# Kernel optimization log

Measured on AMD Instinct MI355X. Metric: run time of the kernel, lower is better.

The kernel has to match this reference:

```python
import jax, jax.numpy as jnp
import numpy as np

B, T, E, H = 256, 256, 384, 64

def setup_inputs() -> dict:
    key = jax.random.key(0)
    ks = jax.random.split(key, 4)
    s = 1.0 / np.sqrt(E)
    return {
        "x":  jax.random.normal(ks[0], (B, T, E), dtype=jnp.float32),
        "Wq": jax.random.normal(ks[1], (E, H), dtype=jnp.float32) * s,
        "bq": jnp.zeros((H,), dtype=jnp.float32),
        "Wk": jax.random.normal(ks[2], (E, H), dtype=jnp.float32) * s,
        "bk": jnp.zeros((H,), dtype=jnp.float32),
        "Wv": jax.random.normal(ks[3], (E, H), dtype=jnp.float32) * s,
        "bv": jnp.zeros((H,), dtype=jnp.float32),
    }

def reference(x, Wq, bq, Wk, bk, Wv, bv):
    # QKV projections: [B,T,E] @ [E,H] -> [B,T,H]
    q = x @ Wq + bq
    k = x @ Wk + bk
    v = x @ Wv + bv
    # attention scores (NOTE: original has no 1/sqrt(d) scaling)
    wei = jnp.einsum('bth,bsh->bts', q, k)  # [B,T,T]
    causal = jnp.tril(jnp.ones((T, T), dtype=bool))
    wei = jnp.where(causal, wei, -jnp.inf)
    wei = jax.nn.softmax(wei, axis=-1)
    # dropout is identity in eval mode
    out = jnp.einsum('bts,bsh->bth', wei, v)  # [B,T,H]
    return out
```

## Files before the change

kernel.cpp:

```cpp
#include <hip/hip_runtime.h>
#include <math.h>

#define Bb 256
#define Tt 256
#define Ee 384
#define Hh 64

typedef __attribute__((ext_vector_type(8))) short bf16x8;
typedef __attribute__((ext_vector_type(4))) float f32x4;
typedef __attribute__((ext_vector_type(4))) unsigned int u32x4;

__device__ inline short f2bf(float f) {
    unsigned u = __float_as_uint(f);
    u += 0x7FFFu + ((u >> 16) & 1);
    return (short)(u >> 16);
}
__device__ inline float bf2f(short s) {
    return __uint_as_float(((unsigned)(unsigned short)s) << 16);
}
__device__ inline unsigned cvt_pk_bf16(float a, float b) {
    unsigned r;
    asm("v_cvt_pk_bf16_f32 %0, %1, %2" : "=v"(r) : "v"(a), "v"(b));
    return r;
}

#define MFMA16(a, b, c) __builtin_amdgcn_mfma_f32_16x16x32_bf16((a), (b), (c), 0, 0, 0)

#define WLO_OFF 147456

#define BB0 65536
#define K_HI 0
#define K_LO 32768
#define VF   65536
#define QH   98304
#define QL   116736
#define PBASE 98304
#define SMEM_BYTES 135168

__global__ __launch_bounds__(256) void prep_w(
    const float* __restrict__ Wq, const float* __restrict__ Wk,
    const float* __restrict__ Wv, unsigned char* __restrict__ wsp)
{
    int u = blockIdx.x * 256 + threadIdx.x;
    if (u >= 9216) return;
    int frag = u >> 6;
    int lu   = u & 63;
    int ec   = frag / 12, tct = frag - ec * 12;
    int koct = lu >> 4, n = lu & 15;
    int col  = tct * 16 + n;
    const float* Wm = (col < 64) ? Wq : ((col < 128) ? Wk : Wv);
    int c = col & 63;
    bf16x8 hi8, lo8;
    #pragma unroll
    for (int j = 0; j < 8; ++j) {
        float v = Wm[(ec * 32 + koct * 8 + j) * 64 + c];
        short h = f2bf(v);
        hi8[j] = h;
        lo8[j] = f2bf(v - bf2f(h));
    }
    *reinterpret_cast<bf16x8*>(wsp + frag * 1024 + lu * 16) = hi8;
    *reinterpret_cast<bf16x8*>(wsp + WLO_OFF + frag * 1024 + lu * 16) = lo8;
}

__global__ __launch_bounds__(1024) void head_fused(
    const float* __restrict__ x,
    const float* __restrict__ bq, const float* __restrict__ bk,
    const float* __restrict__ bv,
    const unsigned char* __restrict__ wsp,
    float* __restrict__ out)
{
    __shared__ __align__(16) unsigned char smem[SMEM_BYTES];

    const int b    = blockIdx.x;
    const int tid  = threadIdx.x;
    const int w    = tid >> 6;
    const int lane = tid & 63;
    const int quad = lane >> 4;
    const int nl   = lane & 15;
    const int ri   = w >> 2;
    const int cj   = w & 3;

    f32x4 acc[4][3];
    #pragma unroll
    for (int i = 0; i < 4; ++i)
        #pragma unroll
        for (int j = 0; j < 3; ++j) acc[i][j] = (f32x4){0,0,0,0};

    const float4* x4 = reinterpret_cast<const float4*>(x + (size_t)b * Tt * Ee);

    auto bgld = [&](int ecn) {
        if (w < 12) {
            int p = ecn & 1;
            const unsigned char* ghi = wsp + (size_t)(ecn * 12 + w) * 1024 + (size_t)lane * 16;
            const unsigned char* glo = ghi + WLO_OFF;
            __builtin_amdgcn_global_load_lds(
                (const __attribute__((address_space(1))) unsigned*)ghi,
                (__attribute__((address_space(3))) unsigned*)(smem + BB0 + p * 24576 + w * 1024),
                16, 0, 0);
            __builtin_amdgcn_global_load_lds(
                (const __attribute__((address_space(1))) unsigned*)glo,
                (__attribute__((address_space(3))) unsigned*)(smem + BB0 + p * 24576 + 12288 + w * 1024),
                16, 0, 0);
        }
    };

    const int pt = tid & 255;
    const float4* xp = x4 + pt * 96;
    unsigned char* adst = smem + (pt >> 4) * 1024 + (pt & 15) * 16;

    auto stageA = [&](int ecsrc, int nb) {
        float4 px[8];
        const float4* xr_ = xp + ecsrc * 8;
        #pragma unroll
        for (int j = 0; j < 8; ++j) px[j] = xr_[j];
        #pragma unroll
        for (int ko = 0; ko < 4; ++ko) {
            float v0 = px[2*ko+0].x, v1 = px[2*ko+0].y,
                  v2 = px[2*ko+0].z, v3 = px[2*ko+0].w,
                  v4 = px[2*ko+1].x, v5 = px[2*ko+1].y,
                  v6 = px[2*ko+1].z, v7 = px[2*ko+1].w;
            unsigned h0 = cvt_pk_bf16(v0, v1);
            unsigned h1 = cvt_pk_bf16(v2, v3);
            unsigned h2 = cvt_pk_bf16(v4, v5);
            unsigned h3 = cvt_pk_bf16(v6, v7);
            unsigned l0 = cvt_pk_bf16(v0 - __uint_as_float(h0 << 16),
                                      v1 - __uint_as_float(h0 & 0xFFFF0000u));
            unsigned l1 = cvt_pk_bf16(v2 - __uint_as_float(h1 << 16),
                                      v3 - __uint_as_float(h1 & 0xFFFF0000u));
            unsigned l2 = cvt_pk_bf16(v4 - __uint_as_float(h2 << 16),
                                      v5 - __uint_as_float(h2 & 0xFFFF0000u));
            unsigned l3 = cvt_pk_bf16(v6 - __uint_as_float(h3 << 16),
                                      v7 - __uint_as_float(h3 & 0xFFFF0000u));
            u32x4 hv = {h0, h1, h2, h3};
            u32x4 lv = {l0, l1, l2, l3};
            *reinterpret_cast<u32x4*>(adst + nb + ko * 256) = hv;
            *reinterpret_cast<u32x4*>(adst + nb + 16384 + ko * 256) = lv;
        }
    };

    bgld(0);
    if (w >= 12) stageA(0, 0);

    for (int ec = 0; ec < 12; ++ec) {
        __syncthreads();
        if (w < 12) {
            if (ec < 11) bgld(ec + 1);
        } else {
            if (ec < 11) stageA(ec + 1, (1 - (ec & 1)) * 32768);
        }

        const int ab = (ec & 1) * 32768;
        const int bb = BB0 + (ec & 1) * 24576;
        bf16x8 bh[3], bl[3];
        #pragma unroll
        for (int ct = 0; ct < 3; ++ct) {
            int o = bb + (cj * 3 + ct) * 1024 + lane * 16;
            bh[ct] = *reinterpret_cast<bf16x8*>(smem + o);
            bl[ct] = *reinterpret_cast<bf16x8*>(smem + o + 12288);
        }
        #pragma unroll
        for (int rt = 0; rt < 4; ++rt) {
            int ao = ab + (4 * ri + rt) * 1024 + lane * 16;
            bf16x8 ah = *reinterpret_cast<bf16x8*>(smem + ao);
            bf16x8 al = *reinterpret_cast<bf16x8*>(smem + ao + 16384);
            #pragma unroll
            for (int ct = 0; ct < 3; ++ct) {
                acc[rt][ct] = MFMA16(ah, bh[ct], acc[rt][ct]);
                acc[rt][ct] = MFMA16(al, bh[ct], acc[rt][ct]);
                acc[rt][ct] = MFMA16(ah, bl[ct], acc[rt][ct]);
            }
        }
    }
    __syncthreads();

    #pragma unroll
    for (int ct = 0; ct < 3; ++ct) {
        int col = (cj * 3 + ct) * 16 + nl;
        float bias = (col < 64) ? bq[col] : (col < 128 ? bk[col - 64] : bv[col - 128]);
        #pragma unroll
        for (int rt = 0; rt < 4; ++rt)
            #pragma unroll
            for (int r = 0; r < 4; ++r) acc[rt][ct][r] += bias;
    }

    #pragma unroll
    for (int ct = 0; ct < 3; ++ct) {
        int col = (cj * 3 + ct) * 16 + nl;
        #pragma unroll
        for (int rt = 0; rt < 4; ++rt) {
            #pragma unroll
            for (int r = 0; r < 4; ++r) {
                float val = acc[rt][ct][r];
                int s = ri * 64 + rt * 16 + quad * 4 + r;
                if (col >= 64 && col < 128) {
                    int h = col - 64;
                    int addr = ((s >> 4) * 2 + (h >> 5)) * 1024
                             + ((((h & 31) >> 3) * 16 + (s & 15)) * 8 + (h & 7)) * 2;
                    short hi = f2bf(val);
                    short lo = f2bf(val - bf2f(hi));
                    *reinterpret_cast<short*>(smem + K_HI + addr) = hi;
                    *reinterpret_cast<short*>(smem + K_LO + addr) = lo;
                } else if (col >= 128) {
                    int h = col - 128, sl = s & 31;
                    int addr = ((s >> 5) * 4 + (h >> 4)) * 1024
                             + (((sl >> 3) * 16 + (h & 15)) * 8 + (sl & 7)) * 2;
                    *reinterpret_cast<short*>(smem + VF + addr) = f2bf(val);
                }
            }
        }
    }

    auto writeQhalf = [&]() {
        #pragma unroll
        for (int ct = 0; ct < 3; ++ct) {
            int col = (cj * 3 + ct) * 16 + nl;
            if (col < 64) {
                #pragma unroll
                for (int rt = 0; rt < 4; ++rt) {
                    #pragma unroll
                    for (int r = 0; r < 4; ++r) {
                        float val = acc[rt][ct][r];
                        int s = ri * 64 + rt * 16 + quad * 4 + r;
                        int rloc = s & 127;
                        short hi = f2bf(val);
                        short lo = f2bf(val - bf2f(hi));
                        *reinterpret_cast<short*>(smem + QH + (rloc * 72 + col) * 2) = hi;
                        *reinterpret_cast<short*>(smem + QL + (rloc * 72 + col) * 2) = lo;
                    }
                }
            }
        }
    };
    bf16x8 qh0, qh1, ql0, ql1;
    auto readQ = [&]() {
        int rloc = (16 * w + nl) & 127;
        int base = rloc * 144;
        qh0 = *reinterpret_cast<bf16x8*>(smem + QH + base + quad * 16);
        qh1 = *reinterpret_cast<bf16x8*>(smem + QH + base + 64 + quad * 16);
        ql0 = *reinterpret_cast<bf16x8*>(smem + QL + base + quad * 16);
        ql1 = *reinterpret_cast<bf16x8*>(smem + QL + base + 64 + quad * 16);
    };

    if (ri < 2) writeQhalf();
    __syncthreads();
    if (w < 8) readQ();
    __syncthreads();
    if (ri >= 2) writeQhalf();
    __syncthreads();
    if (w >= 8) readQ();
    __syncthreads();

    f32x4 oacc[4];
    #pragma unroll
    for (int i = 0; i < 4; ++i) oacc[i] = (f32x4){0,0,0,0};
    float lsum = 0.f;
    const int t0 = w * 16;
    unsigned char* pb = smem + PBASE + w * 1344;
    const int npairs = (w >> 1) + 1;

    for (int p = 0; p < npairs; ++p) {
        #pragma unroll
        for (int hf = 0; hf < 2; ++hf) {
            int st = 2 * p + hf;
            f32x4 s0 = (f32x4){0,0,0,0}, s1 = (f32x4){0,0,0,0};
            int kb = st * 2048 + lane * 16;
            bf16x8 kh0 = *reinterpret_cast<bf16x8*>(smem + K_HI + kb);
            bf16x8 kh1 = *reinterpret_cast<bf16x8*>(smem + K_HI + kb + 1024);
            bf16x8 kl0 = *reinterpret_cast<bf16x8*>(smem + K_LO + kb);
            bf16x8 kl1 = *reinterpret_cast<bf16x8*>(smem + K_LO + kb + 1024);
            s0 = MFMA16(qh0, kh0, s0);
            s1 = MFMA16(qh1, kh1, s1);
            s0 = MFMA16(ql0, kh0, s0);
            s1 = MFMA16(ql1, kh1, s1);
            s0 = MFMA16(qh0, kl0, s0);
            s1 = MFMA16(qh1, kl1, s1);
            int sg = st * 16 + nl;
            #pragma unroll
            for (int r = 0; r < 4; ++r) {
                int tg = t0 + quad * 4 + r;
                float sv = s0[r] + s1[r];
                float pv = (sg <= tg) ? __expf(sv) : 0.f;
                *reinterpret_cast<short*>(pb + ((quad * 4 + r) * 40 + hf * 16 + nl) * 2) = f2bf(pv);
            }
        }
        asm volatile("s_waitcnt lgkmcnt(0)" ::: "memory");
        bf16x8 pa = *reinterpret_cast<bf16x8*>(pb + (nl * 40 + quad * 8) * 2);
        float ls = 0.f;
        #pragma unroll
        for (int j = 0; j < 8; ++j) ls += bf2f(pa[j]);
        ls += __shfl_xor(ls, 16);
        ls += __shfl_xor(ls, 32);
        lsum += ls;
        int vb = p * 4096 + lane * 16;
        #pragma unroll
        for (int nt = 0; nt < 4; ++nt) {
            bf16x8 vf = *reinterpret_cast<bf16x8*>(smem + VF + vb + nt * 1024);
            oacc[nt] = MFMA16(pa, vf, oacc[nt]);
        }
    }

    float* lb_ = reinterpret_cast<float*>(pb + 1280);
    if (lane < 16) lb_[lane] = lsum;
    asm volatile("s_waitcnt lgkmcnt(0)" ::: "memory");
    float* ob = out + (size_t)b * Tt * Hh + (size_t)t0 * Hh;
    #pragma unroll
    for (int r = 0; r < 4; ++r) {
        float inv = 1.0f / lb_[quad * 4 + r];
        #pragma unroll
        for (int nt = 0; nt < 4; ++nt)
            ob[(quad * 4 + r) * 64 + nt * 16 + nl] = oacc[nt][r] * inv;
    }
}

extern "C" void kernel_launch(void* const* d_in, const int* in_sizes, int n_in,
                              void* d_out, int out_size, void* d_ws, size_t ws_size,
                              hipStream_t stream) {
    const float* x  = (const float*)d_in[0];
    const float* Wq = (const float*)d_in[1];
    const float* bq = (const float*)d_in[2];
    const float* bk = (const float*)d_in[4];
    const float* Wk = (const float*)d_in[3];
    const float* Wv = (const float*)d_in[5];
    const float* bv = (const float*)d_in[6];
    float* out = (float*)d_out;
    unsigned char* wsp = (unsigned char*)d_ws;
    hipLaunchKernelGGL(prep_w, dim3(36), dim3(256), 0, stream, Wq, Wk, Wv, wsp);
    hipLaunchKernelGGL(head_fused, dim3(Bb), dim3(1024), 0, stream,
                       x, bq, bk, bv, wsp, out);
}
```

Before: 186.3 us.

## Prefetch x one stage ahead, raise MFMA priority, compute softmax sums in registers

Splits the A-staging step into a global load and a convert/write so the producer waves issue the x loads for chunk ec+2 while chunk ec is consumed, hiding global latency. Wraps MFMA blocks in s_setprio to favour matrix issue across waves. Computes softmax row sums from the fp32 probabilities with cross-lane shuffles instead of re-reading the bf16 P tile and storing sums through LDS. This adds register pressure from the held prefetch buffer, and the normaliser now uses unrounded values.

```diff
diff --git a/kernel.cpp b/kernel.cpp
--- a/kernel.cpp
+++ b/kernel.cpp
@@ -107,12 +107,14 @@
     const int pt = tid & 255;
     const float4* xp = x4 + pt * 96;
     unsigned char* adst = smem + (pt >> 4) * 1024 + (pt & 15) * 16;
-
-    auto stageA = [&](int ecsrc, int nb) {
-        float4 px[8];
+    float4 px[8];
+
+    auto loadX = [&](int ecsrc) {
         const float4* xr_ = xp + ecsrc * 8;
         #pragma unroll
         for (int j = 0; j < 8; ++j) px[j] = xr_[j];
+    };
+    auto stageWrite = [&](int nb) {
         #pragma unroll
         for (int ko = 0; ko < 4; ++ko) {
             float v0 = px[2*ko+0].x, v1 = px[2*ko+0].y,
@@ -139,14 +141,19 @@
     };
 
     bgld(0);
-    if (w >= 12) stageA(0, 0);
+    if (w >= 12) {
+        loadX(0);
+        stageWrite(0);
+        loadX(1);
+    }
 
     for (int ec = 0; ec < 12; ++ec) {
         __syncthreads();
         if (w < 12) {
             if (ec < 11) bgld(ec + 1);
         } else {
-            if (ec < 11) stageA(ec + 1, (1 - (ec & 1)) * 32768);
+            if (ec < 11) stageWrite((1 - (ec & 1)) * 32768);
+            if (ec < 10) loadX(ec + 2);
         }
 
         const int ab = (ec & 1) * 32768;
@@ -158,6 +165,7 @@
             bh[ct] = *reinterpret_cast<bf16x8*>(smem + o);
             bl[ct] = *reinterpret_cast<bf16x8*>(smem + o + 12288);
         }
+        __builtin_amdgcn_s_setprio(1);
         #pragma unroll
         for (int rt = 0; rt < 4; ++rt) {
             int ao = ab + (4 * ri + rt) * 1024 + lane * 16;
@@ -170,6 +178,7 @@
                 acc[rt][ct] = MFMA16(ah, bl[ct], acc[rt][ct]);
             }
         }
+        __builtin_amdgcn_s_setprio(0);
     }
     __syncthreads();
 
@@ -253,12 +262,13 @@
     f32x4 oacc[4];
     #pragma unroll
     for (int i = 0; i < 4; ++i) oacc[i] = (f32x4){0,0,0,0};
-    float lsum = 0.f;
+    float lsum4[4] = {0.f, 0.f, 0.f, 0.f};
     const int t0 = w * 16;
     unsigned char* pb = smem + PBASE + w * 1344;
     const int npairs = (w >> 1) + 1;
 
     for (int p = 0; p < npairs; ++p) {
+        float rs[4] = {0.f, 0.f, 0.f, 0.f};
         #pragma unroll
         for (int hf = 0; hf < 2; ++hf) {
             int st = 2 * p + hf;
@@ -268,44 +278,49 @@
             bf16x8 kh1 = *reinterpret_cast<bf16x8*>(smem + K_HI + kb + 1024);
             bf16x8 kl0 = *reinterpret_cast<bf16x8*>(smem + K_LO + kb);
             bf16x8 kl1 = *reinterpret_cast<bf16x8*>(smem + K_LO + kb + 1024);
+            __builtin_amdgcn_s_setprio(1);
             s0 = MFMA16(qh0, kh0, s0);
             s1 = MFMA16(qh1, kh1, s1);
             s0 = MFMA16(ql0, kh0, s0);
             s1 = MFMA16(ql1, kh1, s1);
             s0 = MFMA16(qh0, kl0, s0);
             s1 = MFMA16(qh1, kl1, s1);
+            __builtin_amdgcn_s_setprio(0);
             int sg = st * 16 + nl;
             #pragma unroll
             for (int r = 0; r < 4; ++r) {
                 int tg = t0 + quad * 4 + r;
                 float sv = s0[r] + s1[r];
                 float pv = (sg <= tg) ? __expf(sv) : 0.f;
+                rs[r] += pv;
                 *reinterpret_cast<short*>(pb + ((quad * 4 + r) * 40 + hf * 16 + nl) * 2) = f2bf(pv);
             }
         }
+        #pragma unroll
+        for (int r = 0; r < 4; ++r) {
+            float v = rs[r];
+            v += __shfl_xor(v, 1);
+            v += __shfl_xor(v, 2);
+            v += __shfl_xor(v, 4);
+            v += __shfl_xor(v, 8);
+            lsum4[r] += v;
+        }
         asm volatile("s_waitcnt lgkmcnt(0)" ::: "memory");
         bf16x8 pa = *reinterpret_cast<bf16x8*>(pb + (nl * 40 + quad * 8) * 2);
-        float ls = 0.f;
-        #pragma unroll
-        for (int j = 0; j < 8; ++j) ls += bf2f(pa[j]);
-        ls += __shfl_xor(ls, 16);
-        ls += __shfl_xor(ls, 32);
-        lsum += ls;
         int vb = p * 4096 + lane * 16;
+        __builtin_amdgcn_s_setprio(1);
         #pragma unroll
         for (int nt = 0; nt < 4; ++nt) {
             bf16x8 vf = *reinterpret_cast<bf16x8*>(smem + VF + vb + nt * 1024);
             oacc[nt] = MFMA16(pa, vf, oacc[nt]);
         }
-    }
-
-    float* lb_ = reinterpret_cast<float*>(pb + 1280);
-    if (lane < 16) lb_[lane] = lsum;
-    asm volatile("s_waitcnt lgkmcnt(0)" ::: "memory");
+        __builtin_amdgcn_s_setprio(0);
+    }
+
     float* ob = out + (size_t)b * Tt * Hh + (size_t)t0 * Hh;
     #pragma unroll
     for (int r = 0; r < 4; ++r) {
-        float inv = 1.0f / lb_[quad * 4 + r];
+        float inv = 1.0f / lsum4[r];
         #pragma unroll
         for (int nt = 0; nt < 4; ++nt)
             ob[(quad * 4 + r) * 64 + nt * 16 + nl] = oacc[nt][r] * inv;
@@ -318,8 +333,8 @@
     const float* x  = (const float*)d_in[0];
     const float* Wq = (const float*)d_in[1];
     const float* bq = (const float*)d_in[2];
+    const float* Wk = (const float*)d_in[3];
     const float* bk = (const float*)d_in[4];
-    const float* Wk = (const float*)d_in[3];
     const float* Wv = (const float*)d_in[5];
     const float* bv = (const float*)d_in[6];
     float* out = (float*)d_out;
```

New measurement: 188.1 us. Within noise of the previous version (+1.0%).

## Specialize warps into producers and 12 MFMA consumers with 4x4 tiles

Applied to the files above, without the earlier changes.

The projection stage is reorganized so four producer waves handle both the weight global-to-LDS loads and the x fp32-to-bf16 hi/lo staging, while twelve consumer waves each compute a 64x64 tile (4x4 MFMA tiles) for one of Q, K or V. This removes the per-element column branching in the epilogue, packs bf16 conversions with v_cvt_pk_bf16, and raises MFMA priority during compute. prep_w now goes through LDS so its global reads coalesce. The trade-off is that only four waves now stage all of x, so the producer side may become the bottleneck, and each consumer holds more accumulator registers.

```diff
diff --git a/kernel.cpp b/kernel.cpp
--- a/kernel.cpp
+++ b/kernel.cpp
@@ -23,6 +23,8 @@
     asm("v_cvt_pk_bf16_f32 %0, %1, %2" : "=v"(r) : "v"(a), "v"(b));
     return r;
 }
+__device__ inline float lo16f(unsigned u) { return __uint_as_float(u << 16); }
+__device__ inline float hi16f(unsigned u) { return __uint_as_float(u & 0xFFFF0000u); }
 
 #define MFMA16(a, b, c) __builtin_amdgcn_mfma_f32_16x16x32_bf16((a), (b), (c), 0, 0, 0)
 
@@ -41,23 +43,32 @@
     const float* __restrict__ Wq, const float* __restrict__ Wk,
     const float* __restrict__ Wv, unsigned char* __restrict__ wsp)
 {
-    int u = blockIdx.x * 256 + threadIdx.x;
-    if (u >= 9216) return;
-    int frag = u >> 6;
-    int lu   = u & 63;
-    int ec   = frag / 12, tct = frag - ec * 12;
-    int koct = lu >> 4, n = lu & 15;
-    int col  = tct * 16 + n;
-    const float* Wm = (col < 64) ? Wq : ((col < 128) ? Wk : Wv);
-    int c = col & 63;
+    __shared__ float wlds[32 * 66];
+    const int bid = blockIdx.x;
+    const int ec  = bid / 3, m = bid - ec * 3;
+    const float* Wm = (m == 0) ? Wq : (m == 1 ? Wk : Wv);
+    const int tid = threadIdx.x;
+
+    const float4* src = reinterpret_cast<const float4*>(Wm + ec * 2048) + tid * 2;
+    float4 a = src[0], b = src[1];
+    int f = tid * 8;
+    float* d = wlds + (f >> 6) * 66 + (f & 63);
+    d[0] = a.x; d[1] = a.y; d[2] = a.z; d[3] = a.w;
+    d[4] = b.x; d[5] = b.y; d[6] = b.z; d[7] = b.w;
+    __syncthreads();
+
+    const int tl = tid >> 6, lu = tid & 63;
+    const int koct = lu >> 4, n = lu & 15;
+    const int c = tl * 16 + n;
     bf16x8 hi8, lo8;
     #pragma unroll
     for (int j = 0; j < 8; ++j) {
-        float v = Wm[(ec * 32 + koct * 8 + j) * 64 + c];
+        float v = wlds[(koct * 8 + j) * 66 + c];
         short h = f2bf(v);
         hi8[j] = h;
         lo8[j] = f2bf(v - bf2f(h));
     }
+    const int frag = ec * 12 + m * 4 + tl;
     *reinterpret_cast<bf16x8*>(wsp + frag * 1024 + lu * 16) = hi8;
     *reinterpret_cast<bf16x8*>(wsp + WLO_OFF + frag * 1024 + lu * 16) = lo8;
 }
@@ -77,30 +88,31 @@
     const int lane = tid & 63;
     const int quad = lane >> 4;
     const int nl   = lane & 15;
-    const int ri   = w >> 2;
-    const int cj   = w & 3;
-
-    f32x4 acc[4][3];
+    const bool producer = (w >= 12);
+    const int rg   = w & 3;
+    const int cg   = w >> 2;
+
+    f32x4 acc[4][4];
     #pragma unroll
     for (int i = 0; i < 4; ++i)
         #pragma unroll
-        for (int j = 0; j < 3; ++j) acc[i][j] = (f32x4){0,0,0,0};
+        for (int j = 0; j < 4; ++j) acc[i][j] = (f32x4){0,0,0,0};
 
     const float4* x4 = reinterpret_cast<const float4*>(x + (size_t)b * Tt * Ee);
 
     auto bgld = [&](int ecn) {
-        if (w < 12) {
-            int p = ecn & 1;
-            const unsigned char* ghi = wsp + (size_t)(ecn * 12 + w) * 1024 + (size_t)lane * 16;
-            const unsigned char* glo = ghi + WLO_OFF;
+        int p = ecn & 1;
+        int f0 = (w - 12) * 3;
+        #pragma unroll
+        for (int j = 0; j < 3; ++j) {
+            const unsigned char* g = wsp + (size_t)(ecn * 12 + f0 + j) * 1024 + (size_t)lane * 16;
+            unsigned char* dlds = smem + BB0 + p * 24576 + (f0 + j) * 1024;
             __builtin_amdgcn_global_load_lds(
-                (const __attribute__((address_space(1))) unsigned*)ghi,
-                (__attribute__((address_space(3))) unsigned*)(smem + BB0 + p * 24576 + w * 1024),
-                16, 0, 0);
+                (const __attribute__((address_space(1))) unsigned*)g,
+                (__attribute__((address_space(3))) unsigned*)dlds, 16, 0, 0);
             __builtin_amdgcn_global_load_lds(
-                (const __attribute__((address_space(1))) unsigned*)glo,
-                (__attribute__((address_space(3))) unsigned*)(smem + BB0 + p * 24576 + 12288 + w * 1024),
-                16, 0, 0);
+                (const __attribute__((address_space(1))) unsigned*)(g + WLO_OFF),
+                (__attribute__((address_space(3))) unsigned*)(dlds + 12288), 16, 0, 0);
         }
     };
 
@@ -123,14 +135,10 @@
             unsigned h1 = cvt_pk_bf16(v2, v3);
             unsigned h2 = cvt_pk_bf16(v4, v5);
             unsigned h3 = cvt_pk_bf16(v6, v7);
-            unsigned l0 = cvt_pk_bf16(v0 - __uint_as_float(h0 << 16),
-                                      v1 - __uint_as_float(h0 & 0xFFFF0000u));
-            unsigned l1 = cvt_pk_bf16(v2 - __uint_as_float(h1 << 16),
-                                      v3 - __uint_as_float(h1 & 0xFFFF0000u));
-            unsigned l2 = cvt_pk_bf16(v4 - __uint_as_float(h2 << 16),
-                                      v5 - __uint_as_float(h2 & 0xFFFF0000u));
-            unsigned l3 = cvt_pk_bf16(v6 - __uint_as_float(h3 << 16),
-                                      v7 - __uint_as_float(h3 & 0xFFFF0000u));
+            unsigned l0 = cvt_pk_bf16(v0 - lo16f(h0), v1 - hi16f(h0));
+            unsigned l1 = cvt_pk_bf16(v2 - lo16f(h1), v3 - hi16f(h1));
+            unsigned l2 = cvt_pk_bf16(v4 - lo16f(h2), v5 - hi16f(h2));
+            unsigned l3 = cvt_pk_bf16(v6 - lo16f(h3), v7 - hi16f(h3));
             u32x4 hv = {h0, h1, h2, h3};
             u32x4 lv = {l0, l1, l2, l3};
             *reinterpret_cast<u32x4*>(adst + nb + ko * 256) = hv;
@@ -138,96 +146,122 @@
         }
     };
 
-    bgld(0);
-    if (w >= 12) stageA(0, 0);
+    if (producer) {
+        bgld(0);
+        stageA(0, 0);
+    }
 
     for (int ec = 0; ec < 12; ++ec) {
         __syncthreads();
-        if (w < 12) {
-            if (ec < 11) bgld(ec + 1);
+        if (producer) {
+            if (ec < 11) {
+                bgld(ec + 1);
+                stageA(ec + 1, (1 - (ec & 1)) * 32768);
+            }
         } else {
-            if (ec < 11) stageA(ec + 1, (1 - (ec & 1)) * 32768);
-        }
-
-        const int ab = (ec & 1) * 32768;
-        const int bb = BB0 + (ec & 1) * 24576;
-        bf16x8 bh[3], bl[3];
-        #pragma unroll
-        for (int ct = 0; ct < 3; ++ct) {
-            int o = bb + (cj * 3 + ct) * 1024 + lane * 16;
-            bh[ct] = *reinterpret_cast<bf16x8*>(smem + o);
-            bl[ct] = *reinterpret_cast<bf16x8*>(smem + o + 12288);
-        }
-        #pragma unroll
-        for (int rt = 0; rt < 4; ++rt) {
-            int ao = ab + (4 * ri + rt) * 1024 + lane * 16;
-            bf16x8 ah = *reinterpret_cast<bf16x8*>(smem + ao);
-            bf16x8 al = *reinterpret_cast<bf16x8*>(smem + ao + 16384);
-            #pragma unroll
-            for (int ct = 0; ct < 3; ++ct) {
-                acc[rt][ct] = MFMA16(ah, bh[ct], acc[rt][ct]);
-                acc[rt][ct] = MFMA16(al, bh[ct], acc[rt][ct]);
-                acc[rt][ct] = MFMA16(ah, bl[ct], acc[rt][ct]);
-            }
-        }
-    }
-    __syncthreads();
-
-    #pragma unroll
-    for (int ct = 0; ct < 3; ++ct) {
-        int col = (cj * 3 + ct) * 16 + nl;
-        float bias = (col < 64) ? bq[col] : (col < 128 ? bk[col - 64] : bv[col - 128]);
-        #pragma unroll
-        for (int rt = 0; rt < 4; ++rt)
-            #pragma unroll
-            for (int r = 0; r < 4; ++r) acc[rt][ct][r] += bias;
-    }
-
-    #pragma unroll
-    for (int ct = 0; ct < 3; ++ct) {
-        int col = (cj * 3 + ct) * 16 + nl;
-        #pragma unroll
-        for (int rt = 0; rt < 4; ++rt) {
-            #pragma unroll
-            for (int r = 0; r < 4; ++r) {
-                float val = acc[rt][ct][r];
-                int s = ri * 64 + rt * 16 + quad * 4 + r;
-                if (col >= 64 && col < 128) {
-                    int h = col - 64;
-                    int addr = ((s >> 4) * 2 + (h >> 5)) * 1024
-                             + ((((h & 31) >> 3) * 16 + (s & 15)) * 8 + (h & 7)) * 2;
-                    short hi = f2bf(val);
-                    short lo = f2bf(val - bf2f(hi));
-                    *reinterpret_cast<short*>(smem + K_HI + addr) = hi;
-                    *reinterpret_cast<short*>(smem + K_LO + addr) = lo;
-                } else if (col >= 128) {
-                    int h = col - 128, sl = s & 31;
-                    int addr = ((s >> 5) * 4 + (h >> 4)) * 1024
-                             + (((sl >> 3) * 16 + (h & 15)) * 8 + (sl & 7)) * 2;
-                    *reinterpret_cast<short*>(smem + VF + addr) = f2bf(val);
+            const int ab = (ec & 1) * 32768;
+            const int bb = BB0 + (ec & 1) * 24576;
+            bf16x8 bh[4], bl[4];
+            #pragma unroll
+            for (int ct = 0; ct < 4; ++ct) {
+                int o = bb + (cg * 4 + ct) * 1024 + lane * 16;
+                bh[ct] = *reinterpret_cast<bf16x8*>(smem + o);
+                bl[ct] = *reinterpret_cast<bf16x8*>(smem + o + 12288);
+            }
+            __builtin_amdgcn_s_setprio(1);
+            #pragma unroll
+            for (int rt = 0; rt < 4; ++rt) {
+                int ao = ab + (rg * 4 + rt) * 1024 + lane * 16;
+                bf16x8 ah = *reinterpret_cast<bf16x8*>(smem + ao);
+                bf16x8 al = *reinterpret_cast<bf16x8*>(smem + ao + 16384);
+                #pragma unroll
+                for (int ct = 0; ct < 4; ++ct) {
+                    acc[rt][ct] = MFMA16(ah, bh[ct], acc[rt][ct]);
+                    acc[rt][ct] = MFMA16(al, bh[ct], acc[rt][ct]);
+                    acc[rt][ct] = MFMA16(ah, bl[ct], acc[rt][ct]);
                 }
             }
-        }
-    }
-
-    auto writeQhalf = [&]() {
-        #pragma unroll
-        for (int ct = 0; ct < 3; ++ct) {
-            int col = (cj * 3 + ct) * 16 + nl;
-            if (col < 64) {
+            __builtin_amdgcn_s_setprio(0);
+        }
+    }
+    __syncthreads();
+
+    if (!producer) {
+        const float* bias_m = (cg == 0) ? bq : (cg == 1 ? bk : bv);
+        #pragma unroll
+        for (int ct = 0; ct < 4; ++ct) {
+            float bias = bias_m[ct * 16 + nl];
+            #pragma unroll
+            for (int rt = 0; rt < 4; ++rt)
+                #pragma unroll
+                for (int r = 0; r < 4; ++r) acc[rt][ct][r] += bias;
+        }
+
+        if (cg == 1) {
+            #pragma unroll
+            for (int ct = 0; ct < 4; ++ct) {
+                int h = ct * 16 + nl;
                 #pragma unroll
                 for (int rt = 0; rt < 4; ++rt) {
-                    #pragma unroll
-                    for (int r = 0; r < 4; ++r) {
-                        float val = acc[rt][ct][r];
-                        int s = ri * 64 + rt * 16 + quad * 4 + r;
-                        int rloc = s & 127;
-                        short hi = f2bf(val);
-                        short lo = f2bf(val - bf2f(hi));
-                        *reinterpret_cast<short*>(smem + QH + (rloc * 72 + col) * 2) = hi;
-                        *reinterpret_cast<short*>(smem + QL + (rloc * 72 + col) * 2) = lo;
-                    }
+                    f32x4 v = acc[rt][ct];
+                    unsigned h01 = cvt_pk_bf16(v[0], v[1]);
+                    unsigned h23 = cvt_pk_bf16(v[2], v[3]);
+                    unsigned l01 = cvt_pk_bf16(v[0] - lo16f(h01), v[1] - hi16f(h01));
+                    unsigned l23 = cvt_pk_bf16(v[2] - lo16f(h23), v[3] - hi16f(h23));
+                    int a0 = ((rg * 4 + rt) * 2 + (h >> 5)) * 1024
+                           + ((((h & 31) >> 3) * 16 + quad * 4) * 8 + (h & 7)) * 2;
+                    *reinterpret_cast<short*>(smem + K_HI + a0)      = (short)h01;
+                    *reinterpret_cast<short*>(smem + K_HI + a0 + 16) = (short)(h01 >> 16);
+                    *reinterpret_cast<short*>(smem + K_HI + a0 + 32) = (short)h23;
+                    *reinterpret_cast<short*>(smem + K_HI + a0 + 48) = (short)(h23 >> 16);
+                    *reinterpret_cast<short*>(smem + K_LO + a0)      = (short)l01;
+                    *reinterpret_cast<short*>(smem + K_LO + a0 + 16) = (short)(l01 >> 16);
+                    *reinterpret_cast<short*>(smem + K_LO + a0 + 32) = (short)l23;
+                    *reinterpret_cast<short*>(smem + K_LO + a0 + 48) = (short)(l23 >> 16);
                 }
+            }
+        } else if (cg == 2) {
+            #pragma unroll
+            for (int ct = 0; ct < 4; ++ct) {
+                int h = ct * 16 + nl;
+                #pragma unroll
+                for (int rt = 0; rt < 4; ++rt) {
+                    f32x4 v = acc[rt][ct];
+                    unsigned h01 = cvt_pk_bf16(v[0], v[1]);
+                    unsigned h23 = cvt_pk_bf16(v[2], v[3]);
+                    int s29 = rg * 2 + (rt >> 1);
+                    int slh = (rt & 1) * 2 + (quad >> 1);
+                    int sl7 = (quad & 1) * 4;
+                    int a0 = (s29 * 4 + (h >> 4)) * 1024
+                           + ((slh * 16 + (h & 15)) * 8 + sl7) * 2;
+                    *reinterpret_cast<unsigned*>(smem + VF + a0)     = h01;
+                    *reinterpret_cast<unsigned*>(smem + VF + a0 + 4) = h23;
+                }
+            }
+        }
+    }
+
+    auto writeQhalf = [&]() {
+        #pragma unroll
+        for (int ct = 0; ct < 4; ++ct) {
+            int col = ct * 16 + nl;
+            #pragma unroll
+            for (int rt = 0; rt < 4; ++rt) {
+                f32x4 v = acc[rt][ct];
+                unsigned h01 = cvt_pk_bf16(v[0], v[1]);
+                unsigned h23 = cvt_pk_bf16(v[2], v[3]);
+                unsigned l01 = cvt_pk_bf16(v[0] - lo16f(h01), v[1] - hi16f(h01));
+                unsigned l23 = cvt_pk_bf16(v[2] - lo16f(h23), v[3] - hi16f(h23));
+                int s0 = rg * 64 + rt * 16 + quad * 4;
+                int a0 = ((s0 & 127) * 72 + col) * 2;
+                *reinterpret_cast<short*>(smem + QH + a0)       = (short)h01;
+                *reinterpret_cast<short*>(smem + QH + a0 + 144) = (short)(h01 >> 16);
+                *reinterpret_cast<short*>(smem + QH + a0 + 288) = (short)h23;
+                *reinterpret_cast<short*>(smem + QH + a0 + 432) = (short)(h23 >> 16);
+                *reinterpret_cast<short*>(smem + QL + a0)       = (short)l01;
+                *reinterpret_cast<short*>(smem + QL + a0 + 144) = (short)(l01 >> 16);
+                *reinterpret_cast<short*>(smem + QL + a0 + 288) = (short)l23;
+                *reinterpret_cast<short*>(smem + QL + a0 + 432) = (short)(l23 >> 16);
             }
         }
     };
@@ -241,11 +275,11 @@
         ql1 = *reinterpret_cast<bf16x8*>(smem + QL + base + 64 + quad * 16);
     };
 
-    if (ri < 2) writeQhalf();
+    if (!producer && cg == 0 && rg < 2) writeQhalf();
     __syncthreads();
     if (w < 8) readQ();
     __syncthreads();
-    if (ri >= 2) writeQhalf();
+    if (!producer && cg == 0 && rg >= 2) writeQhalf();
     __syncthreads();
     if (w >= 8) readQ();
     __syncthreads();
@@ -318,8 +352,8 @@
     const float* x  = (const float*)d_in[0];
     const float* Wq = (const float*)d_in[1];
     const float* bq = (const float*)d_in[2];
+    const float* Wk = (const float*)d_in[3];
     const float* bk = (const float*)d_in[4];
-    const float* Wk = (const float*)d_in[3];
     const float* Wv = (const float*)d_in[5];
     const float* bv = (const float*)d_in[6];
     float* out = (float*)d_out;
```

New measurement: 184.0 us. About the same (-1.2%).
